# Performance work log

Hardware: AMD Instinct MI355X
Metric: run time of the kernel (lower is better)

## Reference

```python
import jax, jax.numpy as jnp
import numpy as np

# Production-scale detection head dims
B_TOTAL = 16      # num_tbins(4) * batch_size(4)
NUM_ANCHORS = 100000
NUM_CLASSES = 8


def setup_inputs() -> dict:
    key = jax.random.key(0)
    k1, k2, k3, k4 = jax.random.split(key, 4)
    # anchors [A,4] = (cx, cy, w, h); widths/heights strictly positive
    ctr = jax.random.uniform(k1, (NUM_ANCHORS, 2), jnp.float32) * 512.0
    wh = jax.random.uniform(k2, (NUM_ANCHORS, 2), jnp.float32) * 64.0 + 8.0
    anchors = jnp.concatenate([ctr, wh], axis=-1)
    loc_preds = jax.random.normal(k3, (B_TOTAL, NUM_ANCHORS, 4), jnp.float32)
    # class scores in [0,1] (post-sigmoid semantics)
    cls_preds = jax.nn.sigmoid(jax.random.normal(k4, (B_TOTAL, NUM_ANCHORS, NUM_CLASSES), jnp.float32))
    return {
        "anchors": anchors,
        "loc_preds": loc_preds,
        "cls_preds": cls_preds,
        "varx": 0.1,
        "vary": 0.2,
        "score_thresh": 0.7,
        "batch_size": 4,
    }


def reference(anchors, loc_preds, cls_preds, varx, vary, score_thresh, batch_size):
    """Anchor decode + score-threshold filtering.

    Faithful to BoxDecoder.forward, but jit-compatible: instead of
    boolean-mask compaction into ragged per-(t,i) lists (data-dependent
    shapes), we return the dense [B*A*C, 6] box tensor plus the keep mask
    and batch_index; (mask, batch_index) fully determine the ragged
    targets[t][i] = box_tensor[mask & (batch_index == t*batch_size+i)].
    """
    B, A, C = cls_preds.shape
    # decode: xy = loc[:2]*varx*anchor_wh + anchor_xy ; wh = exp(loc[2:]*vary)*anchor_wh
    xy = loc_preds[..., :2] * varx * anchors[..., 2:] + anchors[..., :2]
    wh = jnp.exp(loc_preds[..., 2:] * vary) * anchors[..., 2:]
    box_preds = jnp.concatenate([xy - wh * 0.5, xy + wh * 0.5], axis=-1)  # [B,A,4]
    # expand boxes over classes, flatten to [B*A*C, ...] (same order as torch view(-1,...))
    boxes = jnp.broadcast_to(box_preds[:, :, None, :], (B, A, C, 4)).reshape(-1, 4)
    scores = cls_preds.reshape(-1)
    # idxs = b*C + c  ->  label = c+1, batch_index = b
    labels = jnp.broadcast_to(jnp.arange(C, dtype=jnp.float32) + 1.0, (B, A, C)).reshape(-1)
    batch_index = jnp.broadcast_to(jnp.arange(B, dtype=jnp.int32)[:, None, None], (B, A, C)).reshape(-1)
    box_tensor = jnp.concatenate([boxes, scores[:, None], labels[:, None]], axis=1)  # [B*A*C, 6]
    mask = scores >= score_thresh  # keep mask (compaction left to consumer / kernel)
    return box_tensor, mask, batch_index
```

## Files before the change

### kernel.cpp

```cpp
#include <hip/hip_runtime.h>
#include <math.h>


#define MAGIC_SHIFT 38

typedef float vfloat4 __attribute__((ext_vector_type(4)));

__global__ __launch_bounds__(256) void box_decode_kernel(
    const float4* __restrict__ anchors,
    const float4* __restrict__ loc,
    const float*  __restrict__ cls,
    const float*  __restrict__ varx_p,
    const float*  __restrict__ vary_p,
    const float*  __restrict__ th_p,
    vfloat4*      __restrict__ out_box4,
    float*        __restrict__ out_mask,
    float*        __restrict__ out_bidx,
    unsigned n4,
    unsigned A, unsigned C,
    unsigned f4_per_t,
    unsigned long long invA,
    unsigned long long invF)
{
    unsigned g = blockIdx.x * 256u + threadIdx.x;
    if (g >= n4) return;

    unsigned t  = (unsigned)(((unsigned long long)g * invF) >> MAGIC_SHIFT);
    unsigned j  = g - t * f4_per_t;
    unsigned b  = (unsigned)(((unsigned long long)t * invA) >> MAGIC_SHIFT);
    unsigned a  = t - b * A;
    unsigned s  = j / 3u;
    unsigned jm = j - s * 3u;

    float varx = *varx_p;
    float vary = *vary_p;
    float th   = *th_p;

    float4 anc = anchors[a];
    float4 lp  = loc[t];

    float x = fmaf(lp.x * varx, anc.z, anc.x);
    float y = fmaf(lp.y * varx, anc.w, anc.y);
    float w = expf(lp.z * vary) * anc.z;
    float h = expf(lp.w * vary) * anc.w;

    float x1 = fmaf(w, -0.5f, x);
    float y1 = fmaf(h, -0.5f, y);
    float x2 = fmaf(w,  0.5f, x);
    float y2 = fmaf(h,  0.5f, y);

    unsigned r0 = t * C + 2u * s;
    float bf = (float)b;

    vfloat4 r;
    if (jm == 0u) {
        r.x = x1; r.y = y1; r.z = x2; r.w = y2;
    } else if (jm == 1u) {
        float sc0 = cls[r0];
        r.x = sc0;
        r.y = (float)(2u * s + 1u);
        r.z = x1; r.w = y1;
        __builtin_nontemporal_store((sc0 >= th) ? 1.0f : 0.0f, &out_mask[r0]);
        __builtin_nontemporal_store(bf, &out_bidx[r0]);
    } else {
        float sc1 = cls[r0 + 1u];
        r.x = x2; r.y = y2;
        r.z = sc1;
        r.w = (float)(2u * s + 2u);
        __builtin_nontemporal_store((sc1 >= th) ? 1.0f : 0.0f, &out_mask[r0 + 1u]);
        __builtin_nontemporal_store(bf, &out_bidx[r0 + 1u]);
    }
    __builtin_nontemporal_store(r, &out_box4[g]);
}

extern "C" void kernel_launch(void* const* d_in, const int* in_sizes, int n_in,
                              void* d_out, int out_size, void* d_ws, size_t ws_size,
                              hipStream_t stream) {
    const float* anchors = (const float*)d_in[0];
    const float* loc     = (const float*)d_in[1];
    const float* cls     = (const float*)d_in[2];
    const float* varx_p  = (const float*)d_in[3];
    const float* vary_p  = (const float*)d_in[4];
    const float* th_p    = (const float*)d_in[5];

    unsigned A = (unsigned)(in_sizes[0] / 4);
    unsigned B = (unsigned)((unsigned)in_sizes[1] / (4u * A));
    unsigned C = (unsigned)((unsigned)in_sizes[2] / (A * B));
    unsigned rows = B * A * C;

    unsigned f4_per_t = (6u * C) / 4u;
    unsigned n4 = rows * 6u / 4u;

    float* out_box  = (float*)d_out;
    float* out_mask = out_box + (size_t)rows * 6;
    float* out_bidx = out_mask + rows;

    unsigned long long invA = ((1ULL << MAGIC_SHIFT) / A) + 1ULL;
    unsigned long long invF = ((1ULL << MAGIC_SHIFT) / f4_per_t) + 1ULL;

    unsigned nb = (n4 + 255u) / 256u;
    box_decode_kernel<<<dim3(nb), dim3(256), 0, stream>>>(
        (const float4*)anchors, (const float4*)loc, cls,
        varx_p, vary_p, th_p,
        (vfloat4*)out_box, out_mask, out_bidx,
        n4, A, C, f4_per_t, invA, invF);
}
```

Baseline: 500.9 us.

## Add cooperative block kernel staging boxes and scores in shared memory for C=8

Adds a specialized kernel for C=8 where each block handles 64 (batch,anchor) pairs. One group of threads decodes each box once and another loads the class scores as float4, both into shared memory. All threads then write the interleaved 6-wide rows plus mask and batch-index outputs as coalesced float4 stores. This removes the redundant per-output-float4 loc/anchor loads and exp work, and replaces scalar mask/bidx stores with vector stores, at the cost of a __syncthreads and shared-memory staging.

```diff
diff --git a/kernel.cpp b/kernel.cpp
--- a/kernel.cpp
+++ b/kernel.cpp
@@ -5,6 +5,113 @@
 #define MAGIC_SHIFT 38
 
 typedef float vfloat4 __attribute__((ext_vector_type(4)));
+
+__global__ __launch_bounds__(256) void box_decode_coop(
+    const vfloat4* __restrict__ anchors,
+    const vfloat4* __restrict__ loc,
+    const vfloat4* __restrict__ cls4,
+    const float*   __restrict__ varx_p,
+    const float*   __restrict__ vary_p,
+    const float*   __restrict__ th_p,
+    vfloat4*       __restrict__ out_box4,
+    vfloat4*       __restrict__ out_mask4,
+    vfloat4*       __restrict__ out_bidx4,
+    unsigned nT, unsigned A,
+    unsigned long long invA)
+{
+    __shared__ vfloat4 s_box[64];
+    __shared__ vfloat4 s_cls4[128];
+    __shared__ float   s_b[64];
+    const float* s_cls = (const float*)s_cls4;
+
+    const unsigned tid = threadIdx.x;
+    const unsigned t0  = blockIdx.x * 64u;
+
+    const float varx = *varx_p;
+    const float vary = *vary_p;
+    const float th   = *th_p;
+
+    if (tid < 64u) {
+        unsigned t = t0 + tid;
+        if (t < nT) {
+            unsigned b = (unsigned)(((unsigned long long)t * invA) >> MAGIC_SHIFT);
+            unsigned a = t - b * A;
+            vfloat4 anc = anchors[a];
+            vfloat4 lp  = __builtin_nontemporal_load(&loc[t]);
+            float x = fmaf(lp.x * varx, anc.z, anc.x);
+            float y = fmaf(lp.y * varx, anc.w, anc.y);
+            float w = expf(lp.z * vary) * anc.z;
+            float h = expf(lp.w * vary) * anc.w;
+            vfloat4 bx;
+            bx.x = fmaf(w, -0.5f, x);
+            bx.y = fmaf(h, -0.5f, y);
+            bx.z = fmaf(w,  0.5f, x);
+            bx.w = fmaf(h,  0.5f, y);
+            s_box[tid] = bx;
+            s_b[tid]   = (float)b;
+        }
+    } else if (tid < 192u) {
+        unsigned i  = tid - 64u;
+        unsigned gi = t0 * 2u + i;
+        if (gi < nT * 2u)
+            s_cls4[i] = __builtin_nontemporal_load(&cls4[gi]);
+    }
+    __syncthreads();
+
+    {
+        const unsigned nt_blk = (nT - t0 < 64u) ? (nT - t0) : 64u;
+        const unsigned lim    = nt_blk * 12u;
+        const unsigned base   = t0 * 12u;
+#pragma unroll
+        for (unsigned k = 0u; k < 3u; ++k) {
+            unsigned lg = k * 256u + tid;
+            if (lg < lim) {
+                unsigned lt = lg / 12u;
+                unsigned j  = lg - lt * 12u;
+                unsigned s  = j / 3u;
+                unsigned jm = j - s * 3u;
+                vfloat4 bx  = s_box[lt];
+                float sc0 = s_cls[lt * 8u + 2u * s];
+                float sc1 = s_cls[lt * 8u + 2u * s + 1u];
+                float l0  = (float)(2u * s + 1u);
+                float l1  = (float)(2u * s + 2u);
+                bool j0 = (jm == 0u);
+                bool j1 = (jm == 1u);
+                vfloat4 r;
+                r.x = j0 ? bx.x : (j1 ? sc0  : bx.z);
+                r.y = j0 ? bx.y : (j1 ? l0   : bx.w);
+                r.z = j0 ? bx.z : (j1 ? bx.x : sc1);
+                r.w = j0 ? bx.w : (j1 ? bx.y : l1);
+                __builtin_nontemporal_store(r, &out_box4[base + lg]);
+            }
+        }
+    }
+
+    {
+        const unsigned nt_blk = (nT - t0 < 64u) ? (nT - t0) : 64u;
+        const unsigned lim    = nt_blk * 2u;
+        const unsigned mbase  = t0 * 2u;
+        if (tid < 128u) {
+            unsigned i = tid;
+            if (i < lim) {
+                vfloat4 c = s_cls4[i];
+                vfloat4 m;
+                m.x = (c.x >= th) ? 1.0f : 0.0f;
+                m.y = (c.y >= th) ? 1.0f : 0.0f;
+                m.z = (c.z >= th) ? 1.0f : 0.0f;
+                m.w = (c.w >= th) ? 1.0f : 0.0f;
+                __builtin_nontemporal_store(m, &out_mask4[mbase + i]);
+            }
+        } else {
+            unsigned i = tid - 128u;
+            if (i < lim) {
+                float bf = s_b[i >> 1];
+                vfloat4 bb = {bf, bf, bf, bf};
+                __builtin_nontemporal_store(bb, &out_bidx4[mbase + i]);
+            }
+        }
+    }
+}
 
 __global__ __launch_bounds__(256) void box_decode_kernel(
     const float4* __restrict__ anchors,
@@ -16,57 +123,41 @@
     vfloat4*      __restrict__ out_box4,
     float*        __restrict__ out_mask,
     float*        __restrict__ out_bidx,
-    unsigned n4,
-    unsigned A, unsigned C,
-    unsigned f4_per_t,
-    unsigned long long invA,
-    unsigned long long invF)
+    unsigned n4, unsigned A, unsigned C, unsigned f4_per_t,
+    unsigned long long invA, unsigned long long invF)
 {
     unsigned g = blockIdx.x * 256u + threadIdx.x;
     if (g >= n4) return;
-
     unsigned t  = (unsigned)(((unsigned long long)g * invF) >> MAGIC_SHIFT);
     unsigned j  = g - t * f4_per_t;
     unsigned b  = (unsigned)(((unsigned long long)t * invA) >> MAGIC_SHIFT);
     unsigned a  = t - b * A;
     unsigned s  = j / 3u;
     unsigned jm = j - s * 3u;
-
-    float varx = *varx_p;
-    float vary = *vary_p;
-    float th   = *th_p;
-
+    float varx = *varx_p, vary = *vary_p, th = *th_p;
     float4 anc = anchors[a];
     float4 lp  = loc[t];
-
     float x = fmaf(lp.x * varx, anc.z, anc.x);
     float y = fmaf(lp.y * varx, anc.w, anc.y);
     float w = expf(lp.z * vary) * anc.z;
     float h = expf(lp.w * vary) * anc.w;
-
     float x1 = fmaf(w, -0.5f, x);
     float y1 = fmaf(h, -0.5f, y);
     float x2 = fmaf(w,  0.5f, x);
     float y2 = fmaf(h,  0.5f, y);
-
     unsigned r0 = t * C + 2u * s;
     float bf = (float)b;
-
     vfloat4 r;
     if (jm == 0u) {
         r.x = x1; r.y = y1; r.z = x2; r.w = y2;
     } else if (jm == 1u) {
         float sc0 = cls[r0];
-        r.x = sc0;
-        r.y = (float)(2u * s + 1u);
-        r.z = x1; r.w = y1;
+        r.x = sc0; r.y = (float)(2u * s + 1u); r.z = x1; r.w = y1;
         __builtin_nontemporal_store((sc0 >= th) ? 1.0f : 0.0f, &out_mask[r0]);
         __builtin_nontemporal_store(bf, &out_bidx[r0]);
     } else {
         float sc1 = cls[r0 + 1u];
-        r.x = x2; r.y = y2;
-        r.z = sc1;
-        r.w = (float)(2u * s + 2u);
+        r.x = x2; r.y = y2; r.z = sc1; r.w = (float)(2u * s + 2u);
         __builtin_nontemporal_store((sc1 >= th) ? 1.0f : 0.0f, &out_mask[r0 + 1u]);
         __builtin_nontemporal_store(bf, &out_bidx[r0 + 1u]);
     }
@@ -86,22 +177,31 @@
     unsigned A = (unsigned)(in_sizes[0] / 4);
     unsigned B = (unsigned)((unsigned)in_sizes[1] / (4u * A));
     unsigned C = (unsigned)((unsigned)in_sizes[2] / (A * B));
-    unsigned rows = B * A * C;
-
-    unsigned f4_per_t = (6u * C) / 4u;
-    unsigned n4 = rows * 6u / 4u;
+    unsigned nT = B * A;
+    unsigned rows = nT * C;
 
     float* out_box  = (float*)d_out;
     float* out_mask = out_box + (size_t)rows * 6;
     float* out_bidx = out_mask + rows;
 
     unsigned long long invA = ((1ULL << MAGIC_SHIFT) / A) + 1ULL;
-    unsigned long long invF = ((1ULL << MAGIC_SHIFT) / f4_per_t) + 1ULL;
-
-    unsigned nb = (n4 + 255u) / 256u;
-    box_decode_kernel<<<dim3(nb), dim3(256), 0, stream>>>(
-        (const float4*)anchors, (const float4*)loc, cls,
-        varx_p, vary_p, th_p,
-        (vfloat4*)out_box, out_mask, out_bidx,
-        n4, A, C, f4_per_t, invA, invF);
+
+    if (C == 8u) {
+        unsigned nb = (nT + 63u) / 64u;
+        box_decode_coop<<<dim3(nb), dim3(256), 0, stream>>>(
+            (const vfloat4*)anchors, (const vfloat4*)loc, (const vfloat4*)cls,
+            varx_p, vary_p, th_p,
+            (vfloat4*)out_box, (vfloat4*)out_mask, (vfloat4*)out_bidx,
+            nT, A, invA);
+    } else {
+        unsigned f4_per_t = (6u * C) / 4u;
+        unsigned n4 = rows * 6u / 4u;
+        unsigned long long invF = ((1ULL << MAGIC_SHIFT) / f4_per_t) + 1ULL;
+        unsigned nb = (n4 + 255u) / 256u;
+        box_decode_kernel<<<dim3(nb), dim3(256), 0, stream>>>(
+            (const float4*)anchors, (const float4*)loc, cls,
+            varx_p, vary_p, th_p,
+            (vfloat4*)out_box, out_mask, out_bidx,
+            n4, A, C, f4_per_t, invA, invF);
+    }
 }
```

Result: faster. 451.1 us (median of 2 runs) (-9.9%).
